# Kernel optimization log

Measured on AMD Instinct MI355X. Metric: run time of the kernel, lower is better.

Reference implementation:

```python
import jax, jax.numpy as jnp
import numpy as np

N, F, B = 200000, 256, 512


def setup_inputs() -> dict:
    key = jax.random.key(0)
    k1, k2 = jax.random.split(key)
    x = jax.random.normal(k1, (N, F), dtype=jnp.float32)
    batch = jnp.sort(jax.random.randint(k2, (N,), 0, B, dtype=jnp.int64))
    p = jnp.ones((1,), dtype=jnp.float32)
    beta = jnp.ones((1,), dtype=jnp.float32)
    return {"x": x, "batch": batch, "p": p, "beta": beta, "bsize": B}


def reference(x, batch, p, beta, bsize):
    # n_nodes: scatter_add of ones_like(x) -> [B, F] (all columns equal the count)
    counts = jax.ops.segment_sum(jnp.ones((x.shape[0],), x.dtype), batch,
                                 num_segments=bsize)          # [B]
    n_nodes = counts[:, None]                                  # broadcast over F

    # scatter_softmax(p * x.detach(), batch) -- softmax within each graph segment
    a = p * jax.lax.stop_gradient(x)                           # [N, F]
    seg_max = jax.ops.segment_max(a, batch, num_segments=bsize)  # [B, F]
    e = jnp.exp(a - seg_max[batch])                            # [N, F]
    denom = jax.ops.segment_sum(e, batch, num_segments=bsize)  # [B, F]
    w = e / denom[batch]                                       # softmax weights

    # weighted segment-sum, then graph-size rescaling
    s = jax.ops.segment_sum(x * w, batch, num_segments=bsize)  # [B, F]
    return s * n_nodes / (1.0 + beta * (n_nodes - 1.0))
```

## Files before the change

kernel.cpp:

```cpp
#include <hip/hip_runtime.h>
#include <math.h>


constexpr int F      = 256;
constexpr int FT     = F / 2;
constexpr int SPLITS = 8;
constexpr int BLOCK  = FT * SPLITS;
constexpr int DEPTH  = 8;

using f32x2 = __attribute__((ext_vector_type(2))) float;

__global__ __launch_bounds__(BLOCK, 8) void genpool_kernel(
    const f32x2* __restrict__ x2,
    const int*   __restrict__ batch,
    const float* __restrict__ p_ptr,
    const float* __restrict__ beta_ptr,
    f32x2*       __restrict__ out2,
    int N)
{
    const int b     = blockIdx.x;
    const int tid   = threadIdx.x;
    const int f2    = tid & (FT - 1);
    const int split = tid >> 7;

    const float p    = p_ptr[0];
    const float beta = beta_ptr[0];

    int lo0 = 0, hi0 = N, lo1 = 0, hi1 = N;
    while (lo0 < hi0 || lo1 < hi1) {
        int m0i = (lo0 + hi0) >> 1;
        int m1i = (lo1 + hi1) >> 1;
        int v0 = (lo0 < hi0) ? batch[m0i] : 0;
        int v1 = (lo1 < hi1) ? batch[m1i] : 0;
        if (lo0 < hi0) { if (v0 < b)     lo0 = m0i + 1; else hi0 = m0i; }
        if (lo1 < hi1) { if (v1 < b + 1) lo1 = m1i + 1; else hi1 = m1i; }
    }
    const int start = lo0;
    const int end   = lo1;

    float d0 = 0.f, d1 = 0.f, s0 = 0.f, s1 = 0.f;

    int i = start + split;
    for (; i + (DEPTH - 1) * SPLITS < end; i += DEPTH * SPLITS) {
        f32x2 v[DEPTH];
#pragma unroll
        for (int k = 0; k < DEPTH; ++k)
            v[k] = __builtin_nontemporal_load(
                       &x2[(size_t)(i + k * SPLITS) * FT + f2]);
#pragma unroll
        for (int k = 0; k < DEPTH; ++k) {
            float w;
            w = __expf(p * v[k][0]); d0 += w; s0 = fmaf(v[k][0], w, s0);
            w = __expf(p * v[k][1]); d1 += w; s1 = fmaf(v[k][1], w, s1);
        }
    }
    for (; i < end; i += SPLITS) {
        f32x2 v = __builtin_nontemporal_load(&x2[(size_t)i * FT + f2]);
        float w;
        w = __expf(p * v[0]); d0 += w; s0 = fmaf(v[0], w, s0);
        w = __expf(p * v[1]); d1 += w; s1 = fmaf(v[1], w, s1);
    }

    __shared__ f32x2 sd[SPLITS][FT];
    __shared__ f32x2 ss[SPLITS][FT];
    f32x2 vd; vd[0] = d0; vd[1] = d1;
    f32x2 vs; vs[0] = s0; vs[1] = s1;
    sd[split][f2] = vd;
    ss[split][f2] = vs;
    __syncthreads();

    if (tid < FT) {
        float D0 = 0.f, D1 = 0.f, S0 = 0.f, S1 = 0.f;
#pragma unroll
        for (int k = 0; k < SPLITS; ++k) {
            f32x2 kd = sd[k][tid];
            f32x2 ks = ss[k][tid];
            D0 += kd[0]; D1 += kd[1];
            S0 += ks[0]; S1 += ks[1];
        }
        const float cnt = (float)(end - start);
        f32x2 o; o[0] = 0.f; o[1] = 0.f;
        if (cnt > 0.f) {
            const float scale = cnt / (1.f + beta * (cnt - 1.f));
            o[0] = S0 / D0 * scale;
            o[1] = S1 / D1 * scale;
        }
        out2[(size_t)b * FT + tid] = o;
    }
}

extern "C" void kernel_launch(void* const* d_in, const int* in_sizes, int n_in,
                              void* d_out, int out_size, void* d_ws, size_t ws_size,
                              hipStream_t stream)
{
    const f32x2* x2    = (const f32x2*)d_in[0];
    const int*   batch = (const int*)d_in[1];
    const float* p     = (const float*)d_in[2];
    const float* beta  = (const float*)d_in[3];
    f32x2* out2 = (f32x2*)d_out;

    const int N = in_sizes[1];
    const int B = out_size / F;

    genpool_kernel<<<B, BLOCK, 0, stream>>>(x2, batch, p, beta, out2, N);
}
```

Baseline: 40.09 us.

## Split segment pooling into row-chunk partial reduction plus segment combine kernel

Replaces the one-block-per-segment kernel with two kernels. The first splits rows into 512 fixed-size chunks, finds up to two segment boundaries per chunk in shared memory, and writes partial softmax denominators, weighted sums and counts for up to three segments to workspace. The second kernel merges the partials for each segment and applies the size rescaling. The aim is even work per block and no per-block binary search over the batch array. In exchange it adds a second launch and a workspace round trip, and it assumes no chunk holds more than three segments; the old kernel is kept as a fallback when chunks or workspace are too large.

New measurement: 42.51 us. +6.0%, slower.

```diff
diff --git a/kernel.cpp b/kernel.cpp
--- a/kernel.cpp
+++ b/kernel.cpp
@@ -6,63 +6,193 @@
 constexpr int FT     = F / 2;
 constexpr int SPLITS = 8;
 constexpr int BLOCK  = FT * SPLITS;
+constexpr int NCHUNK = 512;
+constexpr int MAXCH  = 512;
+constexpr int SLOT   = 3;
 constexpr int DEPTH  = 8;
 
 using f32x2 = __attribute__((ext_vector_type(2))) float;
 
-__global__ __launch_bounds__(BLOCK, 8) void genpool_kernel(
+__global__ __launch_bounds__(BLOCK, 8) void genpool_phase1(
     const f32x2* __restrict__ x2,
     const int*   __restrict__ batch,
     const float* __restrict__ p_ptr,
-    const float* __restrict__ beta_ptr,
-    f32x2*       __restrict__ out2,
-    int N)
-{
-    const int b     = blockIdx.x;
+    int*    __restrict__ tags,
+    int*    __restrict__ cnts,
+    f32x2*  __restrict__ wsD,
+    f32x2*  __restrict__ wsS,
+    int N, int CH)
+{
+    const int c     = blockIdx.x;
     const int tid   = threadIdx.x;
     const int f2    = tid & (FT - 1);
     const int split = tid >> 7;
 
-    const float p    = p_ptr[0];
+    const int r0  = c * CH;
+    const int len = min(N - r0, CH);
+    const float p = p_ptr[0];
+
+    __shared__ int sb[MAXCH];
+    __shared__ int sbound[2];
+    __shared__ f32x2 sd[SLOT][SPLITS][FT];
+    __shared__ f32x2 ss[SLOT][SPLITS][FT];
+
+    if (tid < 2) sbound[tid] = len;
+    for (int i = tid; i < len; i += BLOCK) sb[i] = batch[r0 + i];
+    __syncthreads();
+
+    const bool trans = (tid >= 1 && tid < len && sb[tid] != sb[tid - 1]);
+    if (trans) atomicMin(&sbound[0], tid);
+    __syncthreads();
+    if (trans && tid != sbound[0]) atomicMin(&sbound[1], tid);
+    __syncthreads();
+
+    int st[4];
+    st[0] = 0;
+    st[1] = sbound[0];
+    st[2] = sbound[1];
+    st[3] = len;
+
+#pragma unroll
+    for (int j = 0; j < SLOT; ++j) {
+        const int a = st[j];
+        const int e = st[j + 1];
+
+        float d0 = 0.f, d1 = 0.f, s0 = 0.f, s1 = 0.f;
+
+        int i = a + split;
+        for (; i + (DEPTH - 1) * SPLITS < e; i += DEPTH * SPLITS) {
+            f32x2 v[DEPTH];
+#pragma unroll
+            for (int k = 0; k < DEPTH; ++k)
+                v[k] = __builtin_nontemporal_load(
+                           &x2[(size_t)(r0 + i + k * SPLITS) * FT + f2]);
+#pragma unroll
+            for (int k = 0; k < DEPTH; ++k) {
+                float w;
+                w = __expf(p * v[k][0]); d0 += w; s0 = fmaf(v[k][0], w, s0);
+                w = __expf(p * v[k][1]); d1 += w; s1 = fmaf(v[k][1], w, s1);
+            }
+        }
+        for (; i < e; i += SPLITS) {
+            f32x2 v = __builtin_nontemporal_load(
+                          &x2[(size_t)(r0 + i) * FT + f2]);
+            float w;
+            w = __expf(p * v[0]); d0 += w; s0 = fmaf(v[0], w, s0);
+            w = __expf(p * v[1]); d1 += w; s1 = fmaf(v[1], w, s1);
+        }
+
+        f32x2 vd; vd[0] = d0; vd[1] = d1;
+        f32x2 vs; vs[0] = s0; vs[1] = s1;
+        sd[j][split][f2] = vd;
+        ss[j][split][f2] = vs;
+    }
+    __syncthreads();
+
+    if (tid < SLOT * FT) {
+        const int j = tid >> 7;
+        const int f = tid & (FT - 1);
+        const int a = st[j];
+        const int e = st[j + 1];
+
+        if (a < e) {
+            float D0 = 0.f, D1 = 0.f, S0 = 0.f, S1 = 0.f;
+#pragma unroll
+            for (int k = 0; k < SPLITS; ++k) {
+                f32x2 kd = sd[j][k][f];
+                f32x2 ks = ss[j][k][f];
+                D0 += kd[0]; D1 += kd[1];
+                S0 += ks[0]; S1 += ks[1];
+            }
+            f32x2 vD; vD[0] = D0; vD[1] = D1;
+            f32x2 vS; vS[0] = S0; vS[1] = S1;
+            wsD[((size_t)c * SLOT + j) * FT + f] = vD;
+            wsS[((size_t)c * SLOT + j) * FT + f] = vS;
+            if (f == 0) {
+                tags[c * SLOT + j] = sb[a];
+                cnts[c * SLOT + j] = e - a;
+            }
+        } else if (f == 0) {
+            tags[c * SLOT + j] = -1;
+        }
+    }
+}
+
+__global__ __launch_bounds__(F, 8) void genpool_phase2(
+    const int*   __restrict__ tags,
+    const int*   __restrict__ cnts,
+    const float* __restrict__ wsDf,
+    const float* __restrict__ wsSf,
+    const float* __restrict__ beta_ptr,
+    float*       __restrict__ out)
+{
+    const int b = blockIdx.x;
+    const int f = threadIdx.x;
+    const float beta = beta_ptr[0];
+
+    int lo = 0, hi = NCHUNK;
+    while (lo < hi) {
+        int mid = (lo + hi) >> 1;
+        if (tags[mid * SLOT] <= b) lo = mid + 1; else hi = mid;
+    }
+    int c = lo - 1;
+
+    float D = 0.f, S = 0.f;
+    int   CNT = 0;
+    while (c >= 0) {
+        bool any = false;
+#pragma unroll
+        for (int j = 0; j < SLOT; ++j) {
+            if (tags[c * SLOT + j] == b) {
+                any = true;
+                D   += wsDf[((size_t)c * SLOT + j) * F + f];
+                S   += wsSf[((size_t)c * SLOT + j) * F + f];
+                CNT += cnts[c * SLOT + j];
+            }
+        }
+        if (!any) break;
+        --c;
+    }
+
+    float val = 0.f;
+    if (CNT > 0) {
+        float n = (float)CNT;
+        val = (S / D) * n / (1.f + beta * (n - 1.f));
+    }
+    out[(size_t)b * F + f] = val;
+}
+
+__global__ __launch_bounds__(BLOCK, 8) void genpool_fallback(
+    const f32x2* __restrict__ x2, const int* __restrict__ batch,
+    const float* __restrict__ p_ptr, const float* __restrict__ beta_ptr,
+    f32x2* __restrict__ out2, int N)
+{
+    const int b = blockIdx.x;
+    const int tid = threadIdx.x;
+    const int f2 = tid & (FT - 1);
+    const int split = tid >> 7;
+    const float p = p_ptr[0];
     const float beta = beta_ptr[0];
 
     int lo0 = 0, hi0 = N, lo1 = 0, hi1 = N;
     while (lo0 < hi0 || lo1 < hi1) {
-        int m0i = (lo0 + hi0) >> 1;
-        int m1i = (lo1 + hi1) >> 1;
+        int m0i = (lo0 + hi0) >> 1, m1i = (lo1 + hi1) >> 1;
         int v0 = (lo0 < hi0) ? batch[m0i] : 0;
         int v1 = (lo1 < hi1) ? batch[m1i] : 0;
         if (lo0 < hi0) { if (v0 < b)     lo0 = m0i + 1; else hi0 = m0i; }
         if (lo1 < hi1) { if (v1 < b + 1) lo1 = m1i + 1; else hi1 = m1i; }
     }
-    const int start = lo0;
-    const int end   = lo1;
+    const int start = lo0, end = lo1;
 
     float d0 = 0.f, d1 = 0.f, s0 = 0.f, s1 = 0.f;
-
-    int i = start + split;
-    for (; i + (DEPTH - 1) * SPLITS < end; i += DEPTH * SPLITS) {
-        f32x2 v[DEPTH];
-#pragma unroll
-        for (int k = 0; k < DEPTH; ++k)
-            v[k] = __builtin_nontemporal_load(
-                       &x2[(size_t)(i + k * SPLITS) * FT + f2]);
-#pragma unroll
-        for (int k = 0; k < DEPTH; ++k) {
-            float w;
-            w = __expf(p * v[k][0]); d0 += w; s0 = fmaf(v[k][0], w, s0);
-            w = __expf(p * v[k][1]); d1 += w; s1 = fmaf(v[k][1], w, s1);
-        }
-    }
-    for (; i < end; i += SPLITS) {
+    for (int i = start + split; i < end; i += SPLITS) {
         f32x2 v = __builtin_nontemporal_load(&x2[(size_t)i * FT + f2]);
         float w;
         w = __expf(p * v[0]); d0 += w; s0 = fmaf(v[0], w, s0);
         w = __expf(p * v[1]); d1 += w; s1 = fmaf(v[1], w, s1);
     }
 
-    __shared__ f32x2 sd[SPLITS][FT];
-    __shared__ f32x2 ss[SPLITS][FT];
+    __shared__ f32x2 sd[SPLITS][FT], ss[SPLITS][FT];
     f32x2 vd; vd[0] = d0; vd[1] = d1;
     f32x2 vs; vs[0] = s0; vs[1] = s1;
     sd[split][f2] = vd;
@@ -97,10 +227,26 @@
     const int*   batch = (const int*)d_in[1];
     const float* p     = (const float*)d_in[2];
     const float* beta  = (const float*)d_in[3];
-    f32x2* out2 = (f32x2*)d_out;
+    float* out = (float*)d_out;
 
     const int N = in_sizes[1];
     const int B = out_size / F;
-
-    genpool_kernel<<<B, BLOCK, 0, stream>>>(x2, batch, p, beta, out2, N);
-}
+    const int CH = (N + NCHUNK - 1) / NCHUNK;
+
+    const size_t n_slots = (size_t)NCHUNK * SLOT;
+    const size_t req = n_slots * 4 * 2 + n_slots * F * 4 * 2;
+
+    if (CH <= MAXCH && ws_size >= req) {
+        int*   tg   = (int*)d_ws;
+        int*   cn   = tg + n_slots;
+        float* wsDf = (float*)(cn + n_slots);
+        float* wsSf = wsDf + n_slots * F;
+
+        genpool_phase1<<<NCHUNK, BLOCK, 0, stream>>>(
+            x2, batch, p, tg, cn, (f32x2*)wsDf, (f32x2*)wsSf, N, CH);
+        genpool_phase2<<<B, F, 0, stream>>>(tg, cn, wsDf, wsSf, beta, out);
+    } else {
+        genpool_fallback<<<B, BLOCK, 0, stream>>>(x2, batch, p, beta,
+                                                  (f32x2*)out, N);
+    }
+}
```
